# Performance work log

Hardware: AMD Instinct MI355X
Metric: run time of the kernel (lower is better)

The kernel has to match this reference:

```python
import jax, jax.numpy as jnp
import numpy as np

MARGIN = 1.0


def setup_inputs() -> dict:
    key = jax.random.key(0)
    k1, k2 = jax.random.split(key)
    B, D = 512, 128
    embeddings = jax.random.normal(k1, (B, D), dtype=jnp.float32)
    labels = jax.random.randint(k2, (B,), 0, 8, dtype=jnp.int64)
    return {"embeddings": embeddings, "labels": labels}


def _triplet_loss(embeddings, labels, margin=MARGIN):
    B = embeddings.shape[0]
    # pairwise euclidean distances (cdist p=2)
    sq = jnp.sum(embeddings * embeddings, axis=1)
    d2 = sq[:, None] + sq[None, :] - 2.0 * (embeddings @ embeddings.T)
    dist = jnp.sqrt(jnp.maximum(d2, 0.0))  # [B, B]

    same = labels[:, None] == labels[None, :]
    eye = jnp.eye(B, dtype=bool)
    pos_mask = same & ~eye          # [B, B] valid positives per anchor
    neg_mask = ~same                # [B, B] valid negatives per anchor
    has_neg = jnp.any(neg_mask, axis=1)  # [B]

    rows = jnp.arange(B)
    # hardest negative per anchor (fallback when no semi-hard negative exists)
    hard_idx = jnp.argmin(jnp.where(neg_mask, dist, jnp.inf), axis=1)  # [B]

    keys = jax.random.split(jax.random.key(42), B)  # one key per positive index p

    def step(carry, xs):
        p, k = xs
        loss_sum, cnt = carry
        pos_d = dist[:, p]                               # [B] anchor->positive dist
        valid = pos_mask[:, p] & has_neg                 # anchor i uses p as positive
        # semi-hard: negative strictly between pos_d and pos_d + margin
        sh = neg_mask & (dist > pos_d[:, None]) & (dist < pos_d[:, None] + margin)
        has_sh = jnp.any(sh, axis=1)
        # uniform random choice among semi-hard negatives via gumbel-argmax
        g = jax.random.gumbel(k, (B, B), dtype=jnp.float32)
        sel = jnp.argmax(jnp.where(sh, g, -jnp.inf), axis=1)
        idx = jnp.where(has_sh, sel, hard_idx)           # [B] chosen negative
        neg_d = dist[rows, idx]
        tl = jax.nn.relu(pos_d - neg_d + margin)
        m = valid & (tl > 0)
        loss_sum = loss_sum + jnp.sum(jnp.where(m, tl, 0.0))
        cnt = cnt + jnp.sum(m.astype(jnp.int32))
        return (loss_sum, cnt), None

    init = (jnp.float32(0.0), jnp.int32(0))
    (loss_sum, cnt), _ = jax.lax.scan(step, init, (rows, keys))
    return jnp.where(cnt == 0, jnp.float32(0.0), loss_sum / cnt.astype(jnp.float32))


def reference(embeddings, labels):
    return _triplet_loss(embeddings, labels)
```

## Files before the change

### kernel.cpp

```cpp
#include <hip/hip_runtime.h>
#include <stdint.h>

#define B 512
#define D 128
#define HALFC 131072u
#define SUB 4
#define NSLOT (SUB * 4)
#define NPART (B * SUB)

__device__ __forceinline__ uint32_t rotl32(uint32_t x, uint32_t r) {
  return (x << r) | (x >> (32u - r));
}

__device__ __forceinline__ void threefry2x32(uint32_t k0, uint32_t k1,
                                             uint32_t x0, uint32_t x1,
                                             uint32_t& y0, uint32_t& y1) {
  uint32_t k2 = k0 ^ k1 ^ 0x1BD11BDAu;
  x0 += k0; x1 += k1;
#define TF_R(r) { x0 += x1; x1 = rotl32(x1, r); x1 ^= x0; }
  TF_R(13) TF_R(15) TF_R(26) TF_R(6)
  x0 += k1; x1 += k2 + 1u;
  TF_R(17) TF_R(29) TF_R(16) TF_R(24)
  x0 += k2; x1 += k0 + 2u;
  TF_R(13) TF_R(15) TF_R(26) TF_R(6)
  x0 += k0; x1 += k1 + 3u;
  TF_R(17) TF_R(29) TF_R(16) TF_R(24)
  x0 += k1; x1 += k2 + 4u;
  TF_R(13) TF_R(15) TF_R(26) TF_R(6)
  x0 += k2; x1 += k0 + 5u;
#undef TF_R
  y0 = x0; y1 = x1;
}

__device__ __forceinline__ void threefry2x32_dual(
    uint32_t k0, uint32_t k1, uint32_t a0, uint32_t a1, uint32_t b0,
    uint32_t b1, uint32_t& ya0, uint32_t& ya1, uint32_t& yb0, uint32_t& yb1) {
  uint32_t k2 = k0 ^ k1 ^ 0x1BD11BDAu;
  a0 += k0; a1 += k1; b0 += k0; b1 += k1;
#define TF_R2(r) { a0 += a1; a1 = rotl32(a1, r); a1 ^= a0; \
                   b0 += b1; b1 = rotl32(b1, r); b1 ^= b0; }
  TF_R2(13) TF_R2(15) TF_R2(26) TF_R2(6)
  a0 += k1; a1 += k2 + 1u; b0 += k1; b1 += k2 + 1u;
  TF_R2(17) TF_R2(29) TF_R2(16) TF_R2(24)
  a0 += k2; a1 += k0 + 2u; b0 += k2; b1 += k0 + 2u;
  TF_R2(13) TF_R2(15) TF_R2(26) TF_R2(6)
  a0 += k0; a1 += k1 + 3u; b0 += k0; b1 += k1 + 3u;
  TF_R2(17) TF_R2(29) TF_R2(16) TF_R2(24)
  a0 += k1; a1 += k2 + 4u; b0 += k1; b1 += k2 + 4u;
  TF_R2(13) TF_R2(15) TF_R2(26) TF_R2(6)
  a0 += k2; a1 += k0 + 5u; b0 += k2; b1 += k0 + 5u;
#undef TF_R2
  ya0 = a0; ya1 = a1; yb0 = b0; yb1 = b1;
}

__global__ __launch_bounds__(256) void dist_kernel(
    const float* __restrict__ emb, float* __restrict__ dist,
    uint32_t* __restrict__ keys0, uint32_t* __restrict__ keys1) {
  __shared__ float As[32][132];
  __shared__ float Bs[32][132];
  __shared__ float sqa[32], sqb[32];
  int bid = blockIdx.x;
  int ti = bid >> 4, tj = bid & 15;
  int t = threadIdx.x;

  const float4* ga = reinterpret_cast<const float4*>(emb + (size_t)ti * 32 * D);
  const float4* gb = reinterpret_cast<const float4*>(emb + (size_t)tj * 32 * D);
  #pragma unroll
  for (int k = 0; k < 4; ++k) {
    int idx = t + k * 256;
    int r = idx >> 5;
    int c4 = idx & 31;
    *reinterpret_cast<float4*>(&As[r][c4 * 4]) = ga[idx];
    *reinterpret_cast<float4*>(&Bs[r][c4 * 4]) = gb[idx];
  }
  __syncthreads();

  {
    int row = t >> 2, seg = t & 3;
    const float* src = (row < 32) ? &As[row][seg * 32] : &Bs[row - 32][seg * 32];
    float s = 0.f;
    #pragma unroll
    for (int m = 0; m < 32; ++m) { float v = src[m]; s += v * v; }
    s += __shfl_xor(s, 1);
    s += __shfl_xor(s, 2);
    if (seg == 0) { if (row < 32) sqa[row] = s; else sqb[row - 32] = s; }
  }

  int r = t >> 3, g = t & 7;
  const float4* A4 = reinterpret_cast<const float4*>(&As[r][0]);
  const float4* B0 = reinterpret_cast<const float4*>(&Bs[g][0]);
  const float4* B1 = reinterpret_cast<const float4*>(&Bs[g + 8][0]);
  const float4* B2 = reinterpret_cast<const float4*>(&Bs[g + 16][0]);
  const float4* B3 = reinterpret_cast<const float4*>(&Bs[g + 24][0]);
  float acc0 = 0.f, acc1 = 0.f, acc2 = 0.f, acc3 = 0.f;
  #pragma unroll 8
  for (int k4 = 0; k4 < 32; ++k4) {
    float4 a = A4[k4];
    float4 b0 = B0[k4], b1 = B1[k4], b2 = B2[k4], b3 = B3[k4];
    acc0 += a.x * b0.x + a.y * b0.y + a.z * b0.z + a.w * b0.w;
    acc1 += a.x * b1.x + a.y * b1.y + a.z * b1.z + a.w * b1.w;
    acc2 += a.x * b2.x + a.y * b2.y + a.z * b2.z + a.w * b2.w;
    acc3 += a.x * b3.x + a.y * b3.y + a.z * b3.z + a.w * b3.w;
  }
  __syncthreads();
  float sa = sqa[r];
  float* drow = dist + (size_t)(ti * 32 + r) * B + tj * 32;
  drow[g]      = sqrtf(fmaxf(sa + sqb[g]      - 2.f * acc0, 0.f));
  drow[g + 8]  = sqrtf(fmaxf(sa + sqb[g + 8]  - 2.f * acc1, 0.f));
  drow[g + 16] = sqrtf(fmaxf(sa + sqb[g + 16] - 2.f * acc2, 0.f));
  drow[g + 24] = sqrtf(fmaxf(sa + sqb[g + 24] - 2.f * acc3, 0.f));

  if (bid == 0) {
    #pragma unroll
    for (int pp = 0; pp < 2; ++pp) {
      int p = t + pp * 256;
      uint32_t i0 = 2u * (uint32_t)p, i1 = i0 + 1u;
      uint32_t a0, a1, b0, b1;
      if (p < 256) {
        threefry2x32(0u, 42u, i0, i0 + 512u, a0, a1);
        threefry2x32(0u, 42u, i1, i1 + 512u, b0, b1);
        keys0[p] = a0; keys1[p] = b0;
      } else {
        threefry2x32(0u, 42u, i0 - 512u, i0, a0, a1);
        threefry2x32(0u, 42u, i1 - 512u, i1, b0, b1);
        keys0[p] = a1; keys1[p] = b1;
      }
    }
  }
}

__global__ __launch_bounds__(256) void triplet_kernel(
    const float* __restrict__ dist, const int* __restrict__ labels,
    const uint32_t* __restrict__ keys0, const uint32_t* __restrict__ keys1,
    double* __restrict__ partials, int* __restrict__ pcnt) {
  __shared__ float drow[B];
  __shared__ unsigned short slab[B];
  __shared__ uint2 skeys[B];
  __shared__ unsigned short list_sh[B];
  __shared__ unsigned short cand[4][B];
  __shared__ int nlist_sh;
  __shared__ double lsum[4];
  __shared__ unsigned int lcnt[4];

  int bid = blockIdx.x;
  int i = bid >> 2;
  int sub = bid & 3;
  int t = threadIdx.x;
  slab[t] = (unsigned short)labels[t];
  slab[t + 256] = (unsigned short)labels[t + 256];
  const float* __restrict__ dg = dist + (size_t)i * B;
  drow[t] = dg[t];
  drow[t + 256] = dg[t + 256];
  skeys[t] = make_uint2(keys0[t], keys1[t]);
  skeys[t + 256] = make_uint2(keys0[t + 256], keys1[t + 256]);
  __syncthreads();

  int wave = t >> 6, lane = t & 63;
  unsigned long long lmask_lt = (1ull << lane) - 1ull;
  unsigned short lab_i = slab[i];

  if (wave == 0) {
    int n = 0;
    #pragma unroll
    for (int c = 0; c < 8; ++c) {
      int r = c * 64 + lane;
      bool v = (slab[r] == lab_i);
      unsigned long long mk = __ballot(v);
      if (v) list_sh[n + __popcll(mk & lmask_lt)] = (unsigned short)r;
      n += __popcll(mk);
    }
    if (lane == 0) nlist_sh = (n == B) ? 0 : n;
  }

  float dd8m[8];
  unsigned long long hkey = ~0ull;
  #pragma unroll
  for (int jc = 0; jc < 8; ++jc) {
    int j = jc * 64 + lane;
    float dv = drow[j];
    bool neg = (slab[j] != lab_i);
    dd8m[jc] = neg ? dv : -3.0e38f;
    if (neg) {
      unsigned long long k =
          (((unsigned long long)__float_as_uint(dv)) << 9) | (unsigned)j;
      if (k < hkey) hkey = k;
    }
  }
  #pragma unroll
  for (int off = 32; off; off >>= 1) {
    unsigned long long o = __shfl_xor(hkey, off);
    if (o < hkey) hkey = o;
  }
  int hard = (int)(hkey & 0x1FFu);
  uint32_t rowbase = (uint32_t)((i & 255) * B);
  bool take_hi = (i >= 256);
  __syncthreads();

  int nlist = nlist_sh;
  unsigned short* wcand = cand[wave];
  double wsum = 0.0;
  unsigned int wcnt = 0;

  for (int k = sub * 4 + wave; k < nlist; k += NSLOT) {
    int p = list_sh[k];
    if (p == i) continue;
    p = __builtin_amdgcn_readfirstlane(p);
    uint2 kp = skeys[p];
    float pos_d = drow[p];
    float hiv = pos_d + 1.0f;

    int nc = 0;
    #pragma unroll
    for (int jc = 0; jc < 8; ++jc) {
      float dd = dd8m[jc];
      bool m = (dd > pos_d) && (dd < hiv);
      unsigned long long mk = __ballot(m);
      if (m) wcand[nc + __popcll(mk & lmask_lt)] =
          (unsigned short)(jc * 64 + lane);
      nc += __popcll(mk);
    }

    int idx;
    if (nc > 0) {
      uint32_t best = 0u;
      int ndual = nc >> 7;
      int c = lane;
      for (int it = 0; it < ndual; ++it, c += 128) {
        int j1 = wcand[c];
        int j2 = wcand[c + 64];
        uint32_t ya0, ya1, yb0, yb1;
        threefry2x32_dual(kp.x, kp.y,
                          rowbase + (uint32_t)j1, rowbase + (uint32_t)j1 + HALFC,
                          rowbase + (uint32_t)j2, rowbase + (uint32_t)j2 + HALFC,
                          ya0, ya1, yb0, yb1);
        uint32_t key1 = ((take_hi ? ya1 : ya0) & 0xFFFFFE00u) |
                        (uint32_t)(511 - j1);
        uint32_t key2 = ((take_hi ? yb1 : yb0) & 0xFFFFFE00u) |
                        (uint32_t)(511 - j2);
        if (key1 > best) best = key1;
        if (key2 > best) best = key2;
      }
      int rem = nc & 127;
      if (rem > 64) {
        int j1 = wcand[c];
        int j2 = wcand[c + 64];
        uint32_t ya0, ya1, yb0, yb1;
        threefry2x32_dual(kp.x, kp.y,
                          rowbase + (uint32_t)j1, rowbase + (uint32_t)j1 + HALFC,
                          rowbase + (uint32_t)j2, rowbase + (uint32_t)j2 + HALFC,
                          ya0, ya1, yb0, yb1);
        uint32_t key1 = ((take_hi ? ya1 : ya0) & 0xFFFFFE00u) |
                        (uint32_t)(511 - j1);
        uint32_t key2 = ((take_hi ? yb1 : yb0) & 0xFFFFFE00u) |
                        (uint32_t)(511 - j2);
        if (c < nc && key1 > best) best = key1;
        if (c + 64 < nc && key2 > best) best = key2;
      } else if (rem > 0) {
        if (c < nc) {
          int j = wcand[c];
          uint32_t y0, y1;
          threefry2x32(kp.x, kp.y, rowbase + (uint32_t)j,
                       rowbase + (uint32_t)j + HALFC, y0, y1);
          uint32_t key1 = ((take_hi ? y1 : y0) & 0xFFFFFE00u) |
                          (uint32_t)(511 - j);
          if (key1 > best) best = key1;
        }
      }
      #pragma unroll
      for (int off = 32; off; off >>= 1) {
        uint32_t ob = (uint32_t)__shfl_xor((int)best, off);
        if (ob > best) best = ob;
      }
      idx = 511 - (int)(best & 0x1FFu);
    } else {
      idx = hard;
    }
    float neg_d = drow[idx];
    float tl = pos_d - neg_d + 1.0f;
    if (tl > 0.f) { wsum += (double)tl; wcnt++; }
  }

  if (lane == 0) { lsum[wave] = wsum; lcnt[wave] = wcnt; }
  __syncthreads();
  if (t == 0) {
    partials[bid] = lsum[0] + lsum[1] + lsum[2] + lsum[3];
    pcnt[bid] = (int)(lcnt[0] + lcnt[1] + lcnt[2] + lcnt[3]);
  }
}

__global__ __launch_bounds__(256) void finalize_kernel(
    const double* __restrict__ partials, const int* __restrict__ pcnt,
    float* __restrict__ out) {
  __shared__ double ss[256];
  __shared__ int sc[256];
  int t = threadIdx.x;
  double s = 0.0;
  int c = 0;
  for (int k = t; k < NPART; k += 256) { s += partials[k]; c += pcnt[k]; }
  ss[t] = s; sc[t] = c;
  __syncthreads();
  for (int st = 128; st; st >>= 1) {
    if (t < st) { ss[t] += ss[t + st]; sc[t] += sc[t + st]; }
    __syncthreads();
  }
  if (t == 0) out[0] = sc[0] ? (float)(ss[0] / (double)sc[0]) : 0.0f;
}

extern "C" void kernel_launch(void* const* d_in, const int* in_sizes, int n_in,
                              void* d_out, int out_size, void* d_ws, size_t ws_size,
                              hipStream_t stream) {
  const float* emb = (const float*)d_in[0];
  const int* labels = (const int*)d_in[1];
  float* out = (float*)d_out;
  char* ws = (char*)d_ws;

  float* dist = (float*)ws;
  uint32_t* keys0 = (uint32_t*)(ws + 1048576);
  uint32_t* keys1 = (uint32_t*)(ws + 1048576 + 2048);
  double* partials = (double*)(ws + 1048576 + 4096);
  int* pcnt = (int*)(ws + 1048576 + 4096 + 16384);

  dist_kernel<<<256, 256, 0, stream>>>(emb, dist, keys0, keys1);
  triplet_kernel<<<B * SUB, 256, 0, stream>>>(dist, labels, keys0, keys1,
                                              partials, pcnt);
  finalize_kernel<<<1, 256, 0, stream>>>(partials, pcnt, out);
}
```

Baseline: 38.20 us.

## Use 512-thread triplet blocks, DPP max reduction and prefetch of next anchor

Doubles the triplet block to eight waves and halves the number of sub-blocks per anchor. Each block now loads labels, keys and the distance row with one element per thread, and the per-anchor list and hardest-negative setup runs half as many times. Replaces the shuffle-based wave max with a DPP row-shift/broadcast sequence and software-prefetches the next positive's key and distance. The self-positive is handled by setting pos_d to -2 so it contributes nothing. Larger blocks may reduce occupancy flexibility and leave more idle waves when positive lists are short.

```diff
diff --git a/kernel.cpp b/kernel.cpp
--- a/kernel.cpp
+++ b/kernel.cpp
@@ -4,8 +4,8 @@
 #define B 512
 #define D 128
 #define HALFC 131072u
-#define SUB 4
-#define NSLOT (SUB * 4)
+#define SUB 2
+#define NSLOT (SUB * 8)
 #define NPART (B * SUB)
 
 __device__ __forceinline__ uint32_t rotl32(uint32_t x, uint32_t r) {
@@ -53,6 +53,21 @@
   ya0 = a0; ya1 = a1; yb0 = b0; yb1 = b1;
 }
 
+__device__ __forceinline__ uint32_t dpp_max_all(uint32_t x) {
+  uint32_t t;
+#define DPP_STEP(ctrl) \
+  t = (uint32_t)__builtin_amdgcn_update_dpp(0, (int)x, ctrl, 0xf, 0xf, true); \
+  x = (t > x) ? t : x;
+  DPP_STEP(0x111)
+  DPP_STEP(0x112)
+  DPP_STEP(0x114)
+  DPP_STEP(0x118)
+  DPP_STEP(0x142)
+  DPP_STEP(0x143)
+#undef DPP_STEP
+  return (uint32_t)__builtin_amdgcn_readlane((int)x, 63);
+}
+
 __global__ __launch_bounds__(256) void dist_kernel(
     const float* __restrict__ emb, float* __restrict__ dist,
     uint32_t* __restrict__ keys0, uint32_t* __restrict__ keys1) {
@@ -129,7 +144,7 @@
   }
 }
 
-__global__ __launch_bounds__(256) void triplet_kernel(
+__global__ __launch_bounds__(512) void triplet_kernel(
     const float* __restrict__ dist, const int* __restrict__ labels,
     const uint32_t* __restrict__ keys0, const uint32_t* __restrict__ keys1,
     double* __restrict__ partials, int* __restrict__ pcnt) {
@@ -137,22 +152,18 @@
   __shared__ unsigned short slab[B];
   __shared__ uint2 skeys[B];
   __shared__ unsigned short list_sh[B];
-  __shared__ unsigned short cand[4][B];
+  __shared__ unsigned short cand[8][B];
   __shared__ int nlist_sh;
-  __shared__ double lsum[4];
-  __shared__ unsigned int lcnt[4];
+  __shared__ double lsum[8];
+  __shared__ unsigned int lcnt[8];
 
   int bid = blockIdx.x;
-  int i = bid >> 2;
-  int sub = bid & 3;
+  int i = bid >> 1;
+  int sub = bid & 1;
   int t = threadIdx.x;
   slab[t] = (unsigned short)labels[t];
-  slab[t + 256] = (unsigned short)labels[t + 256];
-  const float* __restrict__ dg = dist + (size_t)i * B;
-  drow[t] = dg[t];
-  drow[t + 256] = dg[t + 256];
+  drow[t] = dist[(size_t)i * B + t];
   skeys[t] = make_uint2(keys0[t], keys1[t]);
-  skeys[t + 256] = make_uint2(keys0[t + 256], keys1[t + 256]);
   __syncthreads();
 
   int wave = t >> 6, lane = t & 63;
@@ -201,12 +212,21 @@
   double wsum = 0.0;
   unsigned int wcnt = 0;
 
-  for (int k = sub * 4 + wave; k < nlist; k += NSLOT) {
-    int p = list_sh[k];
-    if (p == i) continue;
-    p = __builtin_amdgcn_readfirstlane(p);
-    uint2 kp = skeys[p];
-    float pos_d = drow[p];
+#define LOAD_ANCHOR(KK, KP, PD) { \
+    int p_ = list_sh[KK]; \
+    p_ = __builtin_amdgcn_readfirstlane(p_); \
+    KP = skeys[p_]; \
+    PD = (p_ == i) ? -2.0f : drow[p_];  }
+
+  int k = sub * 8 + wave;
+  uint2 kpN; float pdN;
+  if (k < nlist) LOAD_ANCHOR(k, kpN, pdN);
+
+  while (k < nlist) {
+    uint2 kp = kpN;
+    float pos_d = pdN;
+    int kn = k + NSLOT;
+    if (kn < nlist) LOAD_ANCHOR(kn, kpN, pdN);
     float hiv = pos_d + 1.0f;
 
     int nc = 0;
@@ -220,7 +240,7 @@
       nc += __popcll(mk);
     }
 
-    int idx;
+    float tl = -1.0f;
     if (nc > 0) {
       uint32_t best = 0u;
       int ndual = nc >> 7;
@@ -266,25 +286,26 @@
           if (key1 > best) best = key1;
         }
       }
-      #pragma unroll
-      for (int off = 32; off; off >>= 1) {
-        uint32_t ob = (uint32_t)__shfl_xor((int)best, off);
-        if (ob > best) best = ob;
-      }
-      idx = 511 - (int)(best & 0x1FFu);
+      best = dpp_max_all(best);
+      int idx = 511 - (int)(best & 0x1FFu);
+      tl = pos_d - drow[idx] + 1.0f;
     } else {
-      idx = hard;
-    }
-    float neg_d = drow[idx];
-    float tl = pos_d - neg_d + 1.0f;
+      tl = pos_d - drow[hard] + 1.0f;
+    }
     if (tl > 0.f) { wsum += (double)tl; wcnt++; }
-  }
+    k = kn;
+  }
+#undef LOAD_ANCHOR
 
   if (lane == 0) { lsum[wave] = wsum; lcnt[wave] = wcnt; }
   __syncthreads();
   if (t == 0) {
-    partials[bid] = lsum[0] + lsum[1] + lsum[2] + lsum[3];
-    pcnt[bid] = (int)(lcnt[0] + lcnt[1] + lcnt[2] + lcnt[3]);
+    double s = 0.0;
+    unsigned int c = 0;
+    #pragma unroll
+    for (int w = 0; w < 8; ++w) { s += lsum[w]; c += lcnt[w]; }
+    partials[bid] = s;
+    pcnt[bid] = (int)c;
   }
 }
 
@@ -318,10 +339,10 @@
   uint32_t* keys0 = (uint32_t*)(ws + 1048576);
   uint32_t* keys1 = (uint32_t*)(ws + 1048576 + 2048);
   double* partials = (double*)(ws + 1048576 + 4096);
-  int* pcnt = (int*)(ws + 1048576 + 4096 + 16384);
+  int* pcnt = (int*)(ws + 1048576 + 4096 + 8192);
 
   dist_kernel<<<256, 256, 0, stream>>>(emb, dist, keys0, keys1);
-  triplet_kernel<<<B * SUB, 256, 0, stream>>>(dist, labels, keys0, keys1,
+  triplet_kernel<<<B * SUB, 512, 0, stream>>>(dist, labels, keys0, keys1,
                                               partials, pcnt);
   finalize_kernel<<<1, 256, 0, stream>>>(partials, pcnt, out);
 }
```

Result: faster. 37.18 us (-2.7%).
